# Optimization experiments

Hardware: AMD Instinct MI355X
Metric: run time of the kernel (lower is better)

## Reference

```python
import jax, jax.numpy as jnp
import numpy as np

N = 256   # input_size
H = 512   # hidden_size
B = 128   # batch


def _make_masks(n, h):
    # Replicates MADE.create_masks with n_hidden=1
    d_in = np.arange(n)
    d_h = np.arange(h) % (n - 1)
    d_out = np.arange(n) % n - 1  # = arange(n) - 1
    m0 = (d_h[:, None] >= d_in[None, :]).astype(np.float32)   # (H, N)
    m1 = (d_h[:, None] >= d_h[None, :]).astype(np.float32)    # (H, H)
    m2 = (d_out[:, None] >= d_h[None, :]).astype(np.float32)  # (N, H)
    m2 = np.tile(m2, (2, 1))                                   # (2N, H)
    return jnp.asarray(m0), jnp.asarray(m1), jnp.asarray(m2)


def setup_inputs() -> dict:
    key = jax.random.key(0)
    ks = jax.random.split(key, 7)
    s = 0.02
    return {
        "z": jax.random.normal(ks[0], (B, N), jnp.float32),
        "w0": jax.random.normal(ks[1], (H, N), jnp.float32) * s,
        "b0": jax.random.normal(ks[2], (H,), jnp.float32) * s,
        "w1": jax.random.normal(ks[3], (H, H), jnp.float32) * s,
        "b1": jax.random.normal(ks[4], (H,), jnp.float32) * s,
        "w2": jax.random.normal(ks[5], (2 * N, H), jnp.float32) * s,
        "b2": jax.random.normal(ks[6], (2 * N,), jnp.float32) * s,
    }


def reference(z, w0, b0, w1, b1, w2, b2):
    m0, m1, m2 = _make_masks(N, H)
    mw0 = m0 * w0
    mw1 = m1 * w1
    mw2 = m2 * w2

    def net(x):
        h = jax.nn.relu(x @ mw0.T + b0)
        h = jax.nn.relu(h @ mw1.T + b1)
        return h @ mw2.T + b2  # (B, 2N)

    def step(carry, i):
        x, log_det = carry
        out = net(x)
        mu = out[:, i]          # (B,)
        alpha = out[:, N + i]   # (B,)
        x = x.at[:, i].set(mu + z[:, i] * jnp.exp(alpha))
        return (x, log_det + alpha), None

    x0 = jnp.zeros_like(z)
    ld0 = jnp.zeros((z.shape[0],), z.dtype)
    (x, log_det), _ = jax.lax.scan(step, (x0, ld0), jnp.arange(N))
    return x, -log_det
```

## Files before the change

kernel.cpp:

```cpp
#include <hip/hip_runtime.h>

#define NN 256
#define HH 512
#define BB 128

__global__ void made_prep(const float* __restrict__ w0,
                          const float* __restrict__ w1,
                          const float* __restrict__ w2,
                          float* __restrict__ w0t,
                          float* __restrict__ w1t,
                          float* __restrict__ w2m) {
    int idx = blockIdx.x * blockDim.x + threadIdx.x;
    if (idx < NN * HH) {
        int i = idx >> 9, j = idx & (HH - 1);
        w0t[idx] = ((j % 255) >= i) ? w0[j * NN + i] : 0.f;
    }
    if (idx < HH * HH) {
        int j = idx >> 9, k = idx & (HH - 1);
        w1t[idx] = ((k % 255) >= (j % 255)) ? w1[k * HH + j] : 0.f;
    }
    if (idx < 2 * NN * HH) {
        int o = idx >> 9, k = idx & (HH - 1);
        int base = o & (NN - 1);
        w2m[idx] = ((k % 255) < base) ? w2[idx] : 0.f;
    }
}

struct R8 { float v[8]; };

__device__ __forceinline__ void ld8(R8& d, const float* __restrict__ p, int off) {
    float4 a = *(const float4*)(p + off);
    float4 b = *(const float4*)(p + off + 4);
    d.v[0] = a.x; d.v[1] = a.y; d.v[2] = a.z; d.v[3] = a.w;
    d.v[4] = b.x; d.v[5] = b.y; d.v[6] = b.z; d.v[7] = b.w;
}

__device__ __forceinline__ float rl_f(float v, int lane) {
    return __int_as_float(__builtin_amdgcn_readlane(__float_as_int(v), lane));
}

#define DPP_ADD(v, ctrl, rm) \
    ((v) + __int_as_float(__builtin_amdgcn_update_dpp(0, __float_as_int(v), (ctrl), (rm), 0xf, false)))

__device__ __forceinline__ void reduce2(float& pm, float& pa) {
    pm = DPP_ADD(pm, 0x111, 0xf);  pa = DPP_ADD(pa, 0x111, 0xf);
    pm = DPP_ADD(pm, 0x112, 0xf);  pa = DPP_ADD(pa, 0x112, 0xf);
    pm = DPP_ADD(pm, 0x114, 0xf);  pa = DPP_ADD(pa, 0x114, 0xf);
    pm = DPP_ADD(pm, 0x118, 0xf);  pa = DPP_ADD(pa, 0x118, 0xf);
    pm = DPP_ADD(pm, 0x142, 0xa);  pa = DPP_ADD(pa, 0x142, 0xa);
    pm = DPP_ADD(pm, 0x143, 0xc);  pa = DPP_ADD(pa, 0x143, 0xc);
}

__global__ __launch_bounds__(64)
void made_seq64(const float* __restrict__ z,
                const float* __restrict__ b0g,
                const float* __restrict__ b1g,
                const float* __restrict__ b2g,
                const float* __restrict__ w0t,
                const float* __restrict__ w1t,
                const float* __restrict__ w2m,
                float* __restrict__ out) {
    const int bb  = blockIdx.x;
    const int t   = threadIdx.x;
    const int off = t << 3;

    R8 a0, a1, b2r;
    ld8(a0,  b0g, off);
    ld8(a1,  b1g, off);
    ld8(b2r, b2g, off);
    float4 z4 = *(const float4*)(z + bb * NN + (t << 2));
    float zr[4] = {z4.x, z4.y, z4.z, z4.w};

    R8 w1c0, w1c1;
    ld8(w1c0, w1t + (size_t)510 * HH, off);
    ld8(w1c1, w1t + (size_t)511 * HH, off);

    R8 bw2m[2], bw2a[2], bw0[2], bw1a[2], bw1b[2];
    ld8(bw2m[0], w2m, off);
    ld8(bw2a[0], w2m + (size_t)NN * HH, off);
    ld8(bw0 [0], w0t, off);
    ld8(bw1a[0], w1t, off);
    ld8(bw1b[0], w1t + (size_t)255 * HH, off);

    float ld = 0.f;

    for (int g = 0; g < 32; ++g) {
        #pragma unroll
        for (int r = 0; r < 8; ++r) {
            const int cur = r & 1, nxt = cur ^ 1;
            const int i   = (g << 3) | r;
            const int ipn = (i + 1) & 255;

            ld8(bw2m[nxt], w2m + (size_t)ipn * HH, off);
            ld8(bw2a[nxt], w2m + (size_t)(NN + ipn) * HH, off);
            ld8(bw0 [nxt], w0t + (size_t)ipn * HH, off);
            ld8(bw1a[nxt], w1t + (size_t)ipn * HH, off);
            ld8(bw1b[nxt], w1t + (size_t)(ipn + 255) * HH, off);

            float h[8];
            #pragma unroll
            for (int j = 0; j < 8; ++j) h[j] = fmaxf(a1.v[j], 0.f);

            float pm01 = fmaf(h[1], bw2m[cur].v[1], h[0] * bw2m[cur].v[0]);
            float pm23 = fmaf(h[3], bw2m[cur].v[3], h[2] * bw2m[cur].v[2]);
            float pm45 = fmaf(h[5], bw2m[cur].v[5], h[4] * bw2m[cur].v[4]);
            float pm67 = fmaf(h[7], bw2m[cur].v[7], h[6] * bw2m[cur].v[6]);
            float pm   = (pm01 + pm23) + (pm45 + pm67);

            float pa01 = fmaf(h[1], bw2a[cur].v[1], h[0] * bw2a[cur].v[0]);
            float pa23 = fmaf(h[3], bw2a[cur].v[3], h[2] * bw2a[cur].v[2]);
            float pa45 = fmaf(h[5], bw2a[cur].v[5], h[4] * bw2a[cur].v[4]);
            float pa67 = fmaf(h[7], bw2a[cur].v[7], h[6] * bw2a[cur].v[6]);
            float pa   = (pa01 + pa23) + (pa45 + pa67);

            reduce2(pm, pa);
            float tm = rl_f(pm, 63);
            float ta = rl_f(pa, 63);

            const int sB = (r + 7) & 7;
            const int LB = (r == 0) ? (g + 31) : (g + 32);
            float a0A = rl_f(a0.v[r],          g);
            float w0A = rl_f(bw0[cur].v[r],    g);
            float a0B = rl_f(a0.v[sB],         LB);
            float w0B = rl_f(bw0[cur].v[sB],   LB);

            float mu = tm + rl_f(b2r.v[r], g);
            float al = ta + rl_f(b2r.v[r], g + 32);
            ld += al;
            float zi = rl_f(zr[r & 3], (g << 1) + (r >> 2));
            float xi = fmaf(zi, __expf(al), mu);
            if (t == 0) out[(bb << 8) | i] = xi;

            float h0a = fmaxf(fmaf(xi, w0A, a0A), 0.f);
            float h0b = fmaxf(fmaf(xi, w0B, a0B), 0.f);

            if (r < 2) {
                if (g == 0) {
                    float a0C = rl_f(a0.v[6 + r],       63);
                    float w0C = rl_f(bw0[cur].v[6 + r], 63);
                    float h0c = fmaxf(fmaf(xi, w0C, a0C), 0.f);
                    const R8& wc = (r == 0) ? w1c0 : w1c1;
                    #pragma unroll
                    for (int j = 0; j < 8; ++j)
                        a1.v[j] = fmaf(h0c, wc.v[j], a1.v[j]);
                }
            }

            #pragma unroll
            for (int j = 0; j < 8; ++j)
                a0.v[j] = fmaf(xi, bw0[cur].v[j], a0.v[j]);
            #pragma unroll
            for (int j = 0; j < 8; ++j)
                a1.v[j] = fmaf(h0b, bw1b[cur].v[j], fmaf(h0a, bw1a[cur].v[j], a1.v[j]));
        }
    }

    if (t == 0) out[BB * NN + bb] = -ld;
}

__global__ __launch_bounds__(256)
void made_seq_fb(const float* __restrict__ z,
                 const float* __restrict__ w0, const float* __restrict__ b0,
                 const float* __restrict__ w1, const float* __restrict__ b1,
                 const float* __restrict__ w2, const float* __restrict__ b2,
                 float* __restrict__ out) {
    const int bb = blockIdx.x;
    const int t  = threadIdx.x;
    const int u0 = t, u1 = t + 256;
    const int l0 = u0 % 255, s0 = u0 / 255;
    const int l1 = u1 % 255, s1 = u1 / 255;
    const int wave = t >> 6, lane = t & 63;

    __shared__ float red[2][4][2];
    __shared__ float pub[2][3][2];

    float a0_0 = b0[u0], a0_1 = b0[u1];
    float a1_0 = b1[u0], a1_1 = b1[u1];
    float ld = 0.f;

    for (int i = 0; i < NN; ++i) {
        float cw2m0 = (l0 < i) ? w2[i * HH + u0] : 0.f;
        float cw2a0 = (l0 < i) ? w2[(NN + i) * HH + u0] : 0.f;
        float cw2m1 = (l1 < i) ? w2[i * HH + u1] : 0.f;
        float cw2a1 = (l1 < i) ? w2[(NN + i) * HH + u1] : 0.f;
        float cw00  = (l0 >= i) ? w0[u0 * NN + i] : 0.f;
        float cw01  = (l1 >= i) ? w0[u1 * NN + i] : 0.f;
        bool g0 = (l0 >= (i % 255)), g1 = (l1 >= (i % 255));
        float w1a0 = g0 ? w1[u0 * HH + i] : 0.f;
        float w1a1 = g1 ? w1[u1 * HH + i] : 0.f;
        float w1b0 = g0 ? w1[u0 * HH + i + 255] : 0.f;
        float w1b1 = g1 ? w1[u1 * HH + i + 255] : 0.f;

        float h10 = fmaxf(a1_0, 0.f), h11 = fmaxf(a1_1, 0.f);
        float pm = h10 * cw2m0 + h11 * cw2m1;
        float pa = h10 * cw2a0 + h11 * cw2a1;
        #pragma unroll
        for (int offs = 32; offs > 0; offs >>= 1) {
            pm += __shfl_xor(pm, offs);
            pa += __shfl_xor(pa, offs);
        }
        const int bf = i & 1;
        if (lane == 0) { red[bf][wave][0] = pm; red[bf][wave][1] = pa; }
        if (l0 == i) { pub[bf][s0][0] = a0_0; pub[bf][s0][1] = cw00; }
        if (l1 == i) { pub[bf][s1][0] = a0_1; pub[bf][s1][1] = cw01; }
        __syncthreads();

        float mu = b2[i]      + red[bf][0][0] + red[bf][1][0] + red[bf][2][0] + red[bf][3][0];
        float al = b2[NN + i] + red[bf][0][1] + red[bf][1][1] + red[bf][2][1] + red[bf][3][1];
        ld += al;
        float xi = fmaf(z[bb * NN + i], __expf(al), mu);
        if (t == 0) out[bb * NN + i] = xi;

        a0_0 = fmaf(xi, cw00, a0_0);
        a0_1 = fmaf(xi, cw01, a0_1);

        float h0a = fmaxf(fmaf(xi, pub[bf][0][1], pub[bf][0][0]), 0.f);
        float h0b = fmaxf(fmaf(xi, pub[bf][1][1], pub[bf][1][0]), 0.f);
        a1_0 = fmaf(h0a, w1a0, a1_0);
        a1_1 = fmaf(h0a, w1a1, a1_1);
        a1_0 = fmaf(h0b, w1b0, a1_0);
        a1_1 = fmaf(h0b, w1b1, a1_1);
        if (i < 2) {
            float w1c0 = (l0 >= i) ? w1[u0 * HH + i + 510] : 0.f;
            float w1c1 = (l1 >= i) ? w1[u1 * HH + i + 510] : 0.f;
            float h0c = fmaxf(fmaf(xi, pub[bf][2][1], pub[bf][2][0]), 0.f);
            a1_0 = fmaf(h0c, w1c0, a1_0);
            a1_1 = fmaf(h0c, w1c1, a1_1);
        }
        __syncthreads();
    }

    if (t == 0) out[BB * NN + bb] = -ld;
}

extern "C" void kernel_launch(void* const* d_in, const int* in_sizes, int n_in,
                              void* d_out, int out_size, void* d_ws, size_t ws_size,
                              hipStream_t stream) {
    const float* z  = (const float*)d_in[0];
    const float* w0 = (const float*)d_in[1];
    const float* b0 = (const float*)d_in[2];
    const float* w1 = (const float*)d_in[3];
    const float* b1 = (const float*)d_in[4];
    const float* w2 = (const float*)d_in[5];
    const float* b2 = (const float*)d_in[6];
    float* out = (float*)d_out;

    const size_t need = (size_t)(NN * HH + HH * HH + 2 * NN * HH) * sizeof(float);
    if (ws_size >= need) {
        float* w0t = (float*)d_ws;
        float* w1t = w0t + NN * HH;
        float* w2m = w1t + HH * HH;
        made_prep<<<(2 * NN * HH + 255) / 256, 256, 0, stream>>>(w0, w1, w2, w0t, w1t, w2m);
        made_seq64<<<BB, 64, 0, stream>>>(z, b0, b1, b2, w0t, w1t, w2m, out);
    } else {
        made_seq_fb<<<BB, 256, 0, stream>>>(z, w0, b0, w1, b1, w2, b2, out);
    }
}
```

Baseline: 79.48 us.

## Pack per-step weight rows contiguously and deepen prefetch to two steps ahead

The prep kernel now writes the five masked weight rows each step needs (two w2 rows, one w0 column, two w1 columns) into one contiguous 5*H block per step, and the sequential kernel reads them from there. Instead of the single next-step prefetch, two alternating buffers are kept and each field is refilled for step i+2 as soon as it has been consumed, which hides more global-load latency. Output x values are gathered in registers and written once with a float4 store rather than a scalar store every step. The two corner w1 columns are now read directly from w1 with the mask applied. Register pressure rises with 80 buffered floats per lane, and the prep kernel does strided gathers from w0 and w1.

```diff
diff --git a/kernel.cpp b/kernel.cpp
--- a/kernel.cpp
+++ b/kernel.cpp
@@ -3,40 +3,50 @@
 #define NN 256
 #define HH 512
 #define BB 128
-
-__global__ void made_prep(const float* __restrict__ w0,
-                          const float* __restrict__ w1,
-                          const float* __restrict__ w2,
-                          float* __restrict__ w0t,
-                          float* __restrict__ w1t,
-                          float* __restrict__ w2m) {
-    int idx = blockIdx.x * blockDim.x + threadIdx.x;
-    if (idx < NN * HH) {
-        int i = idx >> 9, j = idx & (HH - 1);
-        w0t[idx] = ((j % 255) >= i) ? w0[j * NN + i] : 0.f;
-    }
-    if (idx < HH * HH) {
-        int j = idx >> 9, k = idx & (HH - 1);
-        w1t[idx] = ((k % 255) >= (j % 255)) ? w1[k * HH + j] : 0.f;
-    }
-    if (idx < 2 * NN * HH) {
-        int o = idx >> 9, k = idx & (HH - 1);
-        int base = o & (NN - 1);
-        w2m[idx] = ((k % 255) < base) ? w2[idx] : 0.f;
-    }
-}
-
-struct R8 { float v[8]; };
-
-__device__ __forceinline__ void ld8(R8& d, const float* __restrict__ p, int off) {
-    float4 a = *(const float4*)(p + off);
-    float4 b = *(const float4*)(p + off + 4);
-    d.v[0] = a.x; d.v[1] = a.y; d.v[2] = a.z; d.v[3] = a.w;
-    d.v[4] = b.x; d.v[5] = b.y; d.v[6] = b.z; d.v[7] = b.w;
+#define PKS (5 * HH)
+
+__global__ __launch_bounds__(512)
+void made_prep(const float* __restrict__ w0,
+               const float* __restrict__ w1,
+               const float* __restrict__ w2,
+               float* __restrict__ pk) {
+    const int i = blockIdx.x;
+    const int k = threadIdx.x;
+    const int lev = k % 255;
+    float* row = pk + (size_t)i * PKS;
+    row[k]          = (lev < i)  ? w2[i * HH + k]        : 0.f;
+    row[HH + k]     = (lev < i)  ? w2[(NN + i) * HH + k] : 0.f;
+    row[2*HH + k]   = (lev >= i) ? w0[k * NN + i]        : 0.f;
+    const int l1 = i % 255;
+    row[3*HH + k]   = (lev >= l1) ? w1[k * HH + i]       : 0.f;
+    const int j2 = i + 255;
+    const int l2 = j2 % 255;
+    row[4*HH + k]   = (lev >= l2) ? w1[k * HH + j2]      : 0.f;
+}
+
+struct B10 { float4 q0,q1,q2,q3,q4,q5,q6,q7,q8,q9; };
+
+__device__ __forceinline__ float4 ld4(const float* p) { return *(const float4*)p; }
+
+__device__ __forceinline__ void load_all(B10& b, const float* p, int o8) {
+    b.q0 = ld4(p + o8);          b.q1 = ld4(p + o8 + 4);
+    b.q2 = ld4(p + HH + o8);     b.q3 = ld4(p + HH + o8 + 4);
+    b.q4 = ld4(p + 2*HH + o8);   b.q5 = ld4(p + 2*HH + o8 + 4);
+    b.q6 = ld4(p + 3*HH + o8);   b.q7 = ld4(p + 3*HH + o8 + 4);
+    b.q8 = ld4(p + 4*HH + o8);   b.q9 = ld4(p + 4*HH + o8 + 4);
 }
 
 __device__ __forceinline__ float rl_f(float v, int lane) {
     return __int_as_float(__builtin_amdgcn_readlane(__float_as_int(v), lane));
+}
+
+__device__ __forceinline__ float q45c(const B10& b, int s) {
+    switch (s) {
+        case 0: return b.q4.x; case 1: return b.q4.y;
+        case 2: return b.q4.z; case 3: return b.q4.w;
+        case 4: return b.q5.x; case 5: return b.q5.y;
+        case 6: return b.q5.z; default: return b.q5.w;
+    }
 }
 
 #define DPP_ADD(v, ctrl, rm) \
@@ -51,111 +61,118 @@
     pm = DPP_ADD(pm, 0x143, 0xc);  pa = DPP_ADD(pa, 0x143, 0xc);
 }
 
-__global__ __launch_bounds__(64)
+#define DOT8(res, A, B)  do {                                   \
+    float t01_ = fmaf(h_[1], (A).y, h_[0] * (A).x);             \
+    float t23_ = fmaf(h_[3], (A).w, h_[2] * (A).z);             \
+    float t45_ = fmaf(h_[5], (B).y, h_[4] * (B).x);             \
+    float t67_ = fmaf(h_[7], (B).w, h_[6] * (B).z);             \
+    res = (t01_ + t23_) + (t45_ + t67_);                        \
+} while (0)
+
+#define STEP(g, r, BUF) do {                                                 \
+    const int i_  = ((g) << 3) | (r);                                        \
+    const float* pf_ = pk + (size_t)((i_ + 2) & 255) * PKS;                  \
+    float h_[8];                                                             \
+    h_[0] = fmaxf(a1v[0], 0.f); h_[1] = fmaxf(a1v[1], 0.f);                  \
+    h_[2] = fmaxf(a1v[2], 0.f); h_[3] = fmaxf(a1v[3], 0.f);                  \
+    h_[4] = fmaxf(a1v[4], 0.f); h_[5] = fmaxf(a1v[5], 0.f);                  \
+    h_[6] = fmaxf(a1v[6], 0.f); h_[7] = fmaxf(a1v[7], 0.f);                  \
+    float pm_, pa_;                                                          \
+    DOT8(pm_, BUF.q0, BUF.q1);                                               \
+    DOT8(pa_, BUF.q2, BUF.q3);                                               \
+    BUF.q0 = ld4(pf_ + o8);        BUF.q1 = ld4(pf_ + o8 + 4);               \
+    BUF.q2 = ld4(pf_ + HH + o8);   BUF.q3 = ld4(pf_ + HH + o8 + 4);          \
+    reduce2(pm_, pa_);                                                       \
+    const int sB_ = ((r) + 7) & 7;                                           \
+    const int LB_ = ((r) == 0) ? ((g) + 31) : ((g) + 32);                    \
+    const int zl_ = ((g) << 1) + ((r) >> 2);                                 \
+    float a0A_ = rl_f(a0v[(r)], (g));                                        \
+    float w0A_ = rl_f(q45c(BUF, (r)), (g));                                  \
+    float a0B_ = rl_f(a0v[sB_], LB_);                                        \
+    float w0B_ = rl_f(q45c(BUF, sB_), LB_);                                  \
+    float tm_ = rl_f(pm_, 63), ta_ = rl_f(pa_, 63);                          \
+    float mu_ = tm_ + rl_f(b2v[(r)], (g));                                   \
+    float al_ = ta_ + rl_f(b2v[(r)], (g) + 32);                              \
+    ldacc += al_;                                                            \
+    float zi_ = rl_f(zrv[(r) & 3], zl_);                                     \
+    float xi_ = fmaf(zi_, __expf(al_), mu_);                                 \
+    xo[(r) & 3] = (t == zl_) ? xi_ : xo[(r) & 3];                            \
+    float h0a_ = fmaxf(fmaf(xi_, w0A_, a0A_), 0.f);                          \
+    float h0b_ = fmaxf(fmaf(xi_, w0B_, a0B_), 0.f);                          \
+    if ((r) < 2 && (g) == 0) {          \
+        float a0C_ = rl_f(a0v[6 + (r)], 63);                                 \
+        float w0C_ = rl_f(q45c(BUF, 6 + (r)), 63);                           \
+        float h0c_ = fmaxf(fmaf(xi_, w0C_, a0C_), 0.f);                      \
+        const float* wc_ = ((r) == 0) ? w1c0v : w1c1v;                       \
+        a1v[0] = fmaf(h0c_, wc_[0], a1v[0]); a1v[1] = fmaf(h0c_, wc_[1], a1v[1]); \
+        a1v[2] = fmaf(h0c_, wc_[2], a1v[2]); a1v[3] = fmaf(h0c_, wc_[3], a1v[3]); \
+        a1v[4] = fmaf(h0c_, wc_[4], a1v[4]); a1v[5] = fmaf(h0c_, wc_[5], a1v[5]); \
+        a1v[6] = fmaf(h0c_, wc_[6], a1v[6]); a1v[7] = fmaf(h0c_, wc_[7], a1v[7]); \
+    }                                                                        \
+    a0v[0] = fmaf(xi_, BUF.q4.x, a0v[0]); a0v[1] = fmaf(xi_, BUF.q4.y, a0v[1]); \
+    a0v[2] = fmaf(xi_, BUF.q4.z, a0v[2]); a0v[3] = fmaf(xi_, BUF.q4.w, a0v[3]); \
+    a0v[4] = fmaf(xi_, BUF.q5.x, a0v[4]); a0v[5] = fmaf(xi_, BUF.q5.y, a0v[5]); \
+    a0v[6] = fmaf(xi_, BUF.q5.z, a0v[6]); a0v[7] = fmaf(xi_, BUF.q5.w, a0v[7]); \
+    BUF.q4 = ld4(pf_ + 2*HH + o8); BUF.q5 = ld4(pf_ + 2*HH + o8 + 4);        \
+    a1v[0] = fmaf(h0b_, BUF.q8.x, fmaf(h0a_, BUF.q6.x, a1v[0]));             \
+    a1v[1] = fmaf(h0b_, BUF.q8.y, fmaf(h0a_, BUF.q6.y, a1v[1]));             \
+    a1v[2] = fmaf(h0b_, BUF.q8.z, fmaf(h0a_, BUF.q6.z, a1v[2]));             \
+    a1v[3] = fmaf(h0b_, BUF.q8.w, fmaf(h0a_, BUF.q6.w, a1v[3]));             \
+    a1v[4] = fmaf(h0b_, BUF.q9.x, fmaf(h0a_, BUF.q7.x, a1v[4]));             \
+    a1v[5] = fmaf(h0b_, BUF.q9.y, fmaf(h0a_, BUF.q7.y, a1v[5]));             \
+    a1v[6] = fmaf(h0b_, BUF.q9.z, fmaf(h0a_, BUF.q7.z, a1v[6]));             \
+    a1v[7] = fmaf(h0b_, BUF.q9.w, fmaf(h0a_, BUF.q7.w, a1v[7]));             \
+    BUF.q6 = ld4(pf_ + 3*HH + o8); BUF.q7 = ld4(pf_ + 3*HH + o8 + 4);        \
+    BUF.q8 = ld4(pf_ + 4*HH + o8); BUF.q9 = ld4(pf_ + 4*HH + o8 + 4);        \
+} while (0)
+
+__global__ __launch_bounds__(64, 1)
 void made_seq64(const float* __restrict__ z,
                 const float* __restrict__ b0g,
                 const float* __restrict__ b1g,
                 const float* __restrict__ b2g,
-                const float* __restrict__ w0t,
-                const float* __restrict__ w1t,
-                const float* __restrict__ w2m,
+                const float* __restrict__ w1,
+                const float* __restrict__ pk,
                 float* __restrict__ out) {
-    const int bb  = blockIdx.x;
-    const int t   = threadIdx.x;
-    const int off = t << 3;
-
-    R8 a0, a1, b2r;
-    ld8(a0,  b0g, off);
-    ld8(a1,  b1g, off);
-    ld8(b2r, b2g, off);
-    float4 z4 = *(const float4*)(z + bb * NN + (t << 2));
-    float zr[4] = {z4.x, z4.y, z4.z, z4.w};
-
-    R8 w1c0, w1c1;
-    ld8(w1c0, w1t + (size_t)510 * HH, off);
-    ld8(w1c1, w1t + (size_t)511 * HH, off);
-
-    R8 bw2m[2], bw2a[2], bw0[2], bw1a[2], bw1b[2];
-    ld8(bw2m[0], w2m, off);
-    ld8(bw2a[0], w2m + (size_t)NN * HH, off);
-    ld8(bw0 [0], w0t, off);
-    ld8(bw1a[0], w1t, off);
-    ld8(bw1b[0], w1t + (size_t)255 * HH, off);
-
-    float ld = 0.f;
+    const int bb = blockIdx.x;
+    const int t  = threadIdx.x;
+    const int o8 = t << 3;
+
+    float a0v[8], a1v[8], b2v[8];
+    {
+        float4 a = ld4(b0g + o8), b = ld4(b0g + o8 + 4);
+        a0v[0]=a.x; a0v[1]=a.y; a0v[2]=a.z; a0v[3]=a.w;
+        a0v[4]=b.x; a0v[5]=b.y; a0v[6]=b.z; a0v[7]=b.w;
+        a = ld4(b1g + o8); b = ld4(b1g + o8 + 4);
+        a1v[0]=a.x; a1v[1]=a.y; a1v[2]=a.z; a1v[3]=a.w;
+        a1v[4]=b.x; a1v[5]=b.y; a1v[6]=b.z; a1v[7]=b.w;
+        a = ld4(b2g + o8); b = ld4(b2g + o8 + 4);
+        b2v[0]=a.x; b2v[1]=a.y; b2v[2]=a.z; b2v[3]=a.w;
+        b2v[4]=b.x; b2v[5]=b.y; b2v[6]=b.z; b2v[7]=b.w;
+    }
+    float w1c0v[8], w1c1v[8];
+    #pragma unroll
+    for (int j = 0; j < 8; ++j) {
+        const int k = o8 + j;
+        w1c0v[j] = w1[k * HH + 510];
+        w1c1v[j] = ((k % 255) >= 1) ? w1[k * HH + 511] : 0.f;
+    }
+    float4 z4 = ld4(z + (bb << 8) + (t << 2));
+    float zrv[4] = {z4.x, z4.y, z4.z, z4.w};
+    float xo[4]  = {0.f, 0.f, 0.f, 0.f};
+    float ldacc  = 0.f;
+
+    B10 Ba, Bb;
+    load_all(Ba, pk, o8);
+    load_all(Bb, pk + PKS, o8);
 
     for (int g = 0; g < 32; ++g) {
-        #pragma unroll
-        for (int r = 0; r < 8; ++r) {
-            const int cur = r & 1, nxt = cur ^ 1;
-            const int i   = (g << 3) | r;
-            const int ipn = (i + 1) & 255;
-
-            ld8(bw2m[nxt], w2m + (size_t)ipn * HH, off);
-            ld8(bw2a[nxt], w2m + (size_t)(NN + ipn) * HH, off);
-            ld8(bw0 [nxt], w0t + (size_t)ipn * HH, off);
-            ld8(bw1a[nxt], w1t + (size_t)ipn * HH, off);
-            ld8(bw1b[nxt], w1t + (size_t)(ipn + 255) * HH, off);
-
-            float h[8];
-            #pragma unroll
-            for (int j = 0; j < 8; ++j) h[j] = fmaxf(a1.v[j], 0.f);
-
-            float pm01 = fmaf(h[1], bw2m[cur].v[1], h[0] * bw2m[cur].v[0]);
-            float pm23 = fmaf(h[3], bw2m[cur].v[3], h[2] * bw2m[cur].v[2]);
-            float pm45 = fmaf(h[5], bw2m[cur].v[5], h[4] * bw2m[cur].v[4]);
-            float pm67 = fmaf(h[7], bw2m[cur].v[7], h[6] * bw2m[cur].v[6]);
-            float pm   = (pm01 + pm23) + (pm45 + pm67);
-
-            float pa01 = fmaf(h[1], bw2a[cur].v[1], h[0] * bw2a[cur].v[0]);
-            float pa23 = fmaf(h[3], bw2a[cur].v[3], h[2] * bw2a[cur].v[2]);
-            float pa45 = fmaf(h[5], bw2a[cur].v[5], h[4] * bw2a[cur].v[4]);
-            float pa67 = fmaf(h[7], bw2a[cur].v[7], h[6] * bw2a[cur].v[6]);
-            float pa   = (pa01 + pa23) + (pa45 + pa67);
-
-            reduce2(pm, pa);
-            float tm = rl_f(pm, 63);
-            float ta = rl_f(pa, 63);
-
-            const int sB = (r + 7) & 7;
-            const int LB = (r == 0) ? (g + 31) : (g + 32);
-            float a0A = rl_f(a0.v[r],          g);
-            float w0A = rl_f(bw0[cur].v[r],    g);
-            float a0B = rl_f(a0.v[sB],         LB);
-            float w0B = rl_f(bw0[cur].v[sB],   LB);
-
-            float mu = tm + rl_f(b2r.v[r], g);
-            float al = ta + rl_f(b2r.v[r], g + 32);
-            ld += al;
-            float zi = rl_f(zr[r & 3], (g << 1) + (r >> 2));
-            float xi = fmaf(zi, __expf(al), mu);
-            if (t == 0) out[(bb << 8) | i] = xi;
-
-            float h0a = fmaxf(fmaf(xi, w0A, a0A), 0.f);
-            float h0b = fmaxf(fmaf(xi, w0B, a0B), 0.f);
-
-            if (r < 2) {
-                if (g == 0) {
-                    float a0C = rl_f(a0.v[6 + r],       63);
-                    float w0C = rl_f(bw0[cur].v[6 + r], 63);
-                    float h0c = fmaxf(fmaf(xi, w0C, a0C), 0.f);
-                    const R8& wc = (r == 0) ? w1c0 : w1c1;
-                    #pragma unroll
-                    for (int j = 0; j < 8; ++j)
-                        a1.v[j] = fmaf(h0c, wc.v[j], a1.v[j]);
-                }
-            }
-
-            #pragma unroll
-            for (int j = 0; j < 8; ++j)
-                a0.v[j] = fmaf(xi, bw0[cur].v[j], a0.v[j]);
-            #pragma unroll
-            for (int j = 0; j < 8; ++j)
-                a1.v[j] = fmaf(h0b, bw1b[cur].v[j], fmaf(h0a, bw1a[cur].v[j], a1.v[j]));
-        }
-    }
-
-    if (t == 0) out[BB * NN + bb] = -ld;
+        STEP(g, 0, Ba); STEP(g, 1, Bb); STEP(g, 2, Ba); STEP(g, 3, Bb);
+        STEP(g, 4, Ba); STEP(g, 5, Bb); STEP(g, 6, Ba); STEP(g, 7, Bb);
+    }
+
+    *(float4*)(out + (bb << 8) + (t << 2)) = make_float4(xo[0], xo[1], xo[2], xo[3]);
+    if (t == 0) out[BB * NN + bb] = -ldacc;
 }
 
 __global__ __launch_bounds__(256)
@@ -245,13 +262,11 @@
     const float* b2 = (const float*)d_in[6];
     float* out = (float*)d_out;
 
-    const size_t need = (size_t)(NN * HH + HH * HH + 2 * NN * HH) * sizeof(float);
+    const size_t need = (size_t)NN * PKS * sizeof(float);
     if (ws_size >= need) {
-        float* w0t = (float*)d_ws;
-        float* w1t = w0t + NN * HH;
-        float* w2m = w1t + HH * HH;
-        made_prep<<<(2 * NN * HH + 255) / 256, 256, 0, stream>>>(w0, w1, w2, w0t, w1t, w2m);
-        made_seq64<<<BB, 64, 0, stream>>>(z, b0, b1, b2, w0t, w1t, w2m, out);
+        float* pk = (float*)d_ws;
+        made_prep<<<NN, 512, 0, stream>>>(w0, w1, w2, pk);
+        made_seq64<<<BB, 64, 0, stream>>>(z, b0, b1, b2, w1, pk, out);
     } else {
         made_seq_fb<<<BB, 256, 0, stream>>>(z, w0, b0, w1, b1, w2, b2, out);
     }
```

New measurement: 92.44 us. 16.3% more time.
